# Optimization experiments

Measured on AMD Instinct MI355X. Metric: run time of the kernel, lower is better.

Reference implementation:

```python
import jax, jax.numpy as jnp
import numpy as np

B, T, D, S, H, O = 256, 64, 16, 64, 128, 8

# Tsit5 Butcher tableau (explicit, FSAL; 5th-order solution weights = last stage row)
C_NODES = [0.0, 0.161, 0.327, 0.9, 0.9800255409045097, 1.0, 1.0]
A_TAB = [
    [],
    [0.161],
    [-0.008480655492356989, 0.335480655492357],
    [2.8971530571054935, -6.359448489975075, 4.3622954328695815],
    [5.325864828439257, -11.748883564062828, 7.4955393428898365, -0.09249506636175525],
    [5.86145544294642, -12.92096931784711, 8.159367898576159, -0.071584973281401, -0.028269050394068383],
    [0.09646076681806523, 0.01, 0.4798896504144996, 1.379008574103742, -3.290069515436081, 2.324710524099774],
]
B_SOL = [0.09646076681806523, 0.01, 0.4798896504144996, 1.379008574103742, -3.290069515436081, 2.324710524099774, 0.0]


def setup_inputs() -> dict:
    key = jax.random.key(0)
    ks = jax.random.split(key, 10)
    ts = jnp.linspace(0.0, 1.0, T)
    coeff_d = 0.05 * jax.random.normal(ks[0], (B, T - 1, D), jnp.float32)
    coeff_c = 0.05 * jax.random.normal(ks[1], (B, T - 1, D), jnp.float32)
    coeff_b = 0.2 * jax.random.normal(ks[2], (B, T - 1, D), jnp.float32)
    coeff_a = jax.random.normal(ks[3], (B, T - 1, D), jnp.float32)

    def lin(k, fo, fi):
        s = 1.0 / np.sqrt(fi)
        kw, kb = jax.random.split(k)
        return (jax.random.uniform(kw, (fo, fi), jnp.float32, -s, s),
                jax.random.uniform(kb, (fo,), jnp.float32, -s, s))

    Wi1, bi1 = lin(ks[4], H, D)
    Wi2, bi2 = lin(ks[5], S, H)
    Wf1, bf1 = lin(ks[6], H, S)
    Wf2, bf2 = lin(ks[7], H, H)
    Wf3, bf3 = lin(ks[8], S * D, H)
    Wr, br = lin(ks[9], O, S)
    return dict(ts=ts, coeff_d=coeff_d, coeff_c=coeff_c, coeff_b=coeff_b, coeff_a=coeff_a,
                Wi1=Wi1, bi1=bi1, Wi2=Wi2, bi2=bi2,
                Wf1=Wf1, bf1=bf1, Wf2=Wf2, bf2=bf2, Wf3=Wf3, bf3=bf3, Wr=Wr, br=br)


def _forward(ts, coeff_d, coeff_c, coeff_b, coeff_a,
             Wi1, bi1, Wi2, bi2, Wf1, bf1, Wf2, bf2, Wf3, bf3, Wr, br):
    def vf(y, dxdt):
        # y: (B,S); f(y): (B,S,D) from the MLP (softplus hidden, tanh final); return f(y) @ dx/dt
        h1 = jax.nn.softplus(y @ Wf1.T + bf1)
        h2 = jax.nn.softplus(h1 @ Wf2.T + bf2)
        M = jnp.tanh(h2 @ Wf3.T + bf3).reshape(y.shape[0], S, D)
        return jnp.einsum('bsd,bd->bs', M, dxdt)

    # y0 = initial_mlp(control.evaluate(ts[0])); cubic eval at interval start is coeff_a[:,0]
    x0 = coeff_a[:, 0, :]
    y0 = jax.nn.softplus(x0 @ Wi1.T + bi1) @ Wi2.T + bi2  # (B,S)

    hs = jnp.diff(ts)  # (T-1,)

    def step(y, inp):
        h, cd, cc, cb = inp  # h scalar step size; cd/cc/cb: (B,D) cubic coeffs of this interval
        ks = []
        for j in range(7):
            yj = y
            for m, a in enumerate(A_TAB[j]):
                yj = yj + (h * a) * ks[m]
            frac = C_NODES[j] * h
            dxdt = cb + frac * (2.0 * cc + 3.0 * frac * cd)  # d/dt of cubic interpolation
            ks.append(vf(yj, dxdt))
        y_new = y + h * sum(w * k for w, k in zip(B_SOL, ks))
        return y_new, y_new

    xs = (hs, jnp.swapaxes(coeff_d, 0, 1), jnp.swapaxes(coeff_c, 0, 1), jnp.swapaxes(coeff_b, 0, 1))
    _, ys = jax.lax.scan(step, y0, xs)
    ys = jnp.concatenate([y0[None], ys], axis=0)  # (T,B,S), saved at every ts
    out = ys @ Wr.T + br  # linear readout, identity activation
    return jnp.swapaxes(out, 0, 1)  # (B,T,O)


def reference(ts, coeff_d, coeff_c, coeff_b, coeff_a, Wi1, bi1, Wi2, bi2,
              Wf1, bf1, Wf2, bf2, Wf3, bf3, Wr, br):
    return _forward(ts, coeff_d, coeff_c, coeff_b, coeff_a,
                    Wi1, bi1, Wi2, bi2, Wf1, bf1, Wf2, bf2, Wf3, bf3, Wr, br)
```

## Files before the change

### kernel.cpp

```cpp
#include <hip/hip_runtime.h>
#include <math.h>

typedef _Float16 half_t;
typedef _Float16 half2_t __attribute__((ext_vector_type(2)));
typedef _Float16 half8_t __attribute__((ext_vector_type(8)));
typedef float float4_t __attribute__((ext_vector_type(4)));

#define T_ 64
#define B_ 256
#define D_ 16
#define S_ 64
#define SP_ 68
#define H_ 128
#define O_ 8
#define NSTEP 63
#define NT 512

#define W3_OFF 0
#define W1_OFF 131072
#define W2_OFF 139264
#define WS_HALVES 155648

#define MFMA16(a, b, c) __builtin_amdgcn_mfma_f32_16x16x32_f16(a, b, c, 0, 0, 0)

#if __has_builtin(__builtin_amdgcn_mov_dpp)
#define DPP_ADD(x, ctrl) \
  ((x) + __int_as_float(__builtin_amdgcn_mov_dpp(__float_as_int(x), (ctrl), 0xF, 0xF, true)))
#else
#define DPP_ADD(x, ctrl) ((x) + __shfl_xor((x), (ctrl) == 0xB1 ? 1 : (ctrl) == 0x4E ? 2 : (ctrl) == 0x141 ? 4 : 8))
#endif

__device__ constexpr float AE[6][6] = {
  {0.161f, 0.f, 0.f, 0.f, 0.f, 0.f},
  {-0.008480655492356989f, 0.335480655492357f, 0.f, 0.f, 0.f, 0.f},
  {2.8971530571054935f, -6.359448489975075f, 4.3622954328695815f, 0.f, 0.f, 0.f},
  {5.325864828439257f, -11.748883564062828f, 7.4955393428898365f, -0.09249506636175525f, 0.f, 0.f},
  {5.86145544294642f, -12.92096931784711f, 8.159367898576159f, -0.071584973281401f, -0.028269050394068383f, 0.f},
  {0.09646076681806523f, 0.01f, 0.4798896504144996f, 1.379008574103742f, -3.290069515436081f, 2.324710524099774f}
};
__device__ constexpr float CCn[6] = {0.f, 0.161f, 0.327f, 0.9f, 0.9800255409045097f, 1.f};

__device__ __forceinline__ float softplus_f(float x) {
  return fmaxf(x, 0.f) + __logf(1.f + __expf(-fabsf(x)));
}
__device__ __forceinline__ float tanh_f(float x) {
  float xc = fminf(fmaxf(x, -12.f), 12.f);
  float e = __expf(2.f * xc);
  return (e - 1.f) * __builtin_amdgcn_rcpf(e + 1.f);
}

__global__ __launch_bounds__(256) void convert_kernel(
    const float* __restrict__ Wf1, const float* __restrict__ Wf2,
    const float* __restrict__ Wf3, half_t* __restrict__ wsh)
{
  int q = blockIdx.x * 256 + threadIdx.x;
  if (q < W1_OFF) wsh[q] = (half_t)Wf3[q];
  else if (q < W2_OFF) wsh[q] = (half_t)Wf1[q - W1_OFF];
  else if (q < WS_HALVES) wsh[q] = (half_t)Wf2[q - W2_OFF];
}

__global__ void __launch_bounds__(NT) __attribute__((amdgpu_waves_per_eu(2, 2)))
cde_kernel_mfma(
    const float* __restrict__ ts,
    const float* __restrict__ coeff_d,
    const float* __restrict__ coeff_c,
    const float* __restrict__ coeff_b,
    const float* __restrict__ coeff_a,
    const float* __restrict__ Wi1, const float* __restrict__ bi1,
    const float* __restrict__ Wi2, const float* __restrict__ bi2,
    const float* __restrict__ bf1, const float* __restrict__ bf2,
    const float* __restrict__ bf3,
    const float* __restrict__ Wr, const float* __restrict__ br,
    const half_t* __restrict__ wsh,
    float* __restrict__ out)
{
  __shared__ __align__(16) half_t syj_h[S_];
  __shared__ __align__(16) half_t sh1h[H_];
  __shared__ __align__(16) half_t sh2h[H_];
  __shared__ __align__(16) float shist[T_][SP_];
  __shared__ float sWr[O_ * S_];
  __shared__ float sbr[O_];
  __shared__ float sx0[D_];
  __shared__ float sini[H_];
  __shared__ float shs[T_];

  const int tid = threadIdx.x;
  const int b = blockIdx.x;
  const int w = tid >> 6;
  const int lane = tid & 63;
  const int q = lane >> 4;
  const int c = lane & 15;

  const half_t* __restrict__ w3p = wsh + W3_OFF;
  const half_t* __restrict__ w1p = wsh + W1_OFF;
  const half_t* __restrict__ w2p = wsh + W2_OFF;

  const int n1 = 16 * w + c;
  half8_t bW1[2], bW2[4], bW3[8][4];
  #pragma unroll
  for (int ks = 0; ks < 2; ++ks)
    bW1[ks] = *(const half8_t*)(w1p + n1 * S_ + ks * 32 + q * 8);
  #pragma unroll
  for (int ks = 0; ks < 4; ++ks)
    bW2[ks] = *(const half8_t*)(w2p + n1 * H_ + ks * 32 + q * 8);
  #pragma unroll
  for (int t = 0; t < 8; ++t) {
    const int r = 16 * (8 * w + t) + c;
    #pragma unroll
    for (int ks = 0; ks < 4; ++ks)
      bW3[t][ks] = *(const half8_t*)(w3p + (size_t)r * H_ + ks * 32 + q * 8);
  }
  const float bf1r = bf1[n1];
  const float bf2r = bf2[n1];
  const int s0 = 8 * w + 2 * q;
  const float bf3r0 = bf3[16 * s0 + c];
  const float bf3r1 = bf3[16 * (s0 + 1) + c];

  if (tid < O_ * S_) sWr[tid] = Wr[tid];
  if (tid < O_) sbr[tid] = br[tid];
  if (tid < D_) sx0[tid] = coeff_a[(size_t)b * NSTEP * D_ + tid];
  if (tid < NSTEP) shs[tid] = ts[tid + 1] - ts[tid];
  __syncthreads();
  if (tid < H_) {
    float acc = bi1[tid];
    #pragma unroll
    for (int d = 0; d < D_; ++d) acc += sx0[d] * Wi1[tid * D_ + d];
    sini[tid] = softplus_f(acc);
  }
  __syncthreads();
  if (tid < S_) {
    float acc = bi2[tid];
    for (int h = 0; h < H_; ++h) acc += sini[h] * Wi2[tid * H_ + h];
    shist[0][tid] = acc;
  }
  __syncthreads();

  float yr0 = shist[0][s0];
  float yr1 = shist[0][s0 + 1];
  float kr0[6] = {0.f,0.f,0.f,0.f,0.f,0.f};
  float kr1[6] = {0.f,0.f,0.f,0.f,0.f,0.f};
  if (c == 0) {
    half2_t p; p[0] = (half_t)yr0; p[1] = (half_t)yr1;
    *(half2_t*)(syj_h + s0) = p;
  }
  __syncthreads();

  const float4_t Zv = {0.f, 0.f, 0.f, 0.f};

  for (int t = 0; t < NSTEP; ++t) {
    const float hstep = shs[t];
    const size_t cidx = ((size_t)b * NSTEP + t) * D_ + c;
    const float cbv = coeff_b[cidx];
    const float ccv = coeff_c[cidx];
    const float cdv = coeff_d[cidx];
    float dxj[6];
    #pragma unroll
    for (int j = 0; j < 6; ++j) {
      const float frac = CCn[j] * hstep;
      dxj[j] = cbv + frac * (2.f * ccv + 3.f * frac * cdv);
    }

    #pragma unroll
    for (int j = 0; j < 6; ++j) {
      {
        const half8_t* ap = (const half8_t*)syj_h;
        half8_t a0 = ap[q];
        half8_t a1 = ap[4 + q];
        float4_t acc0 = MFMA16(a0, bW1[0], Zv);
        float4_t acc1 = MFMA16(a1, bW1[1], Zv);
        if (q == 0) sh1h[n1] = (half_t)softplus_f(acc0[0] + acc1[0] + bf1r);
      }
      __syncthreads();

      {
        const half8_t* ap = (const half8_t*)sh1h;
        half8_t a0 = ap[q], a1 = ap[4 + q], a2 = ap[8 + q], a3 = ap[12 + q];
        float4_t accA = MFMA16(a0, bW2[0], Zv);
        float4_t accB = MFMA16(a1, bW2[1], Zv);
        accA = MFMA16(a2, bW2[2], accA);
        accB = MFMA16(a3, bW2[3], accB);
        if (q == 0) sh2h[n1] = (half_t)softplus_f(accA[0] + accB[0] + bf2r);
      }
      __syncthreads();

      {
        const half8_t* ap = (const half8_t*)sh2h;
        half8_t a0 = ap[q], a1 = ap[4 + q], a2 = ap[8 + q], a3 = ap[12 + q];
        float4_t acc3[8];
        #pragma unroll
        for (int tt = 0; tt < 8; ++tt) acc3[tt] = MFMA16(a0, bW3[tt][0], Zv);
        #pragma unroll
        for (int tt = 0; tt < 8; ++tt) acc3[tt] = MFMA16(a1, bW3[tt][1], acc3[tt]);
        #pragma unroll
        for (int tt = 0; tt < 8; ++tt) acc3[tt] = MFMA16(a2, bW3[tt][2], acc3[tt]);
        #pragma unroll
        for (int tt = 0; tt < 8; ++tt) acc3[tt] = MFMA16(a3, bW3[tt][3], acc3[tt]);

        float v0, v1;
        if (q == 0)      { v0 = acc3[0][0]; v1 = acc3[1][0]; }
        else if (q == 1) { v0 = acc3[2][0]; v1 = acc3[3][0]; }
        else if (q == 2) { v0 = acc3[4][0]; v1 = acc3[5][0]; }
        else             { v0 = acc3[6][0]; v1 = acc3[7][0]; }

        const float dx = dxj[j];
        float p0 = tanh_f(v0 + bf3r0) * dx;
        float p1 = tanh_f(v1 + bf3r1) * dx;
        p0 = DPP_ADD(p0, 0xB1);   p1 = DPP_ADD(p1, 0xB1);
        p0 = DPP_ADD(p0, 0x4E);   p1 = DPP_ADD(p1, 0x4E);
        p0 = DPP_ADD(p0, 0x141);  p1 = DPP_ADD(p1, 0x141);
        p0 = DPP_ADD(p0, 0x140);  p1 = DPP_ADD(p1, 0x140);

        kr0[j] = p0;
        kr1[j] = p1;
        float sa0 = AE[j][0] * kr0[0];
        float sa1 = AE[j][0] * kr1[0];
        #pragma unroll
        for (int m = 1; m < 6; ++m) if (m <= j) { sa0 = fmaf(AE[j][m], kr0[m], sa0); sa1 = fmaf(AE[j][m], kr1[m], sa1); }
        float yn0 = fmaf(hstep, sa0, yr0);
        float yn1 = fmaf(hstep, sa1, yr1);
        if (j == 5) { yr0 = yn0; yr1 = yn1; }
        if (c == 0) {
          half2_t p; p[0] = (half_t)yn0; p[1] = (half_t)yn1;
          *(half2_t*)(syj_h + s0) = p;
          if (j == 5) {
            float2 f; f.x = yn0; f.y = yn1;
            *(float2*)(&shist[t + 1][s0]) = f;
          }
        }
      }
      __syncthreads();
    }
  }

  __syncthreads();
  {
    const int tt = tid >> 3;
    const int oo = tid & 7;
    const float4* yp = (const float4*)(&shist[tt][0]);
    const float4* wp = (const float4*)(sWr + oo * S_);
    float a0 = 0.f, a1 = 0.f;
    #pragma unroll
    for (int i = 0; i < 16; i += 2) {
      float4 y0 = yp[i], w0 = wp[i];
      float4 y1 = yp[i + 1], w1 = wp[i + 1];
      a0 += y0.x * w0.x + y0.y * w0.y + y0.z * w0.z + y0.w * w0.w;
      a1 += y1.x * w1.x + y1.y * w1.y + y1.z * w1.z + y1.w * w1.w;
    }
    out[((size_t)b * T_ + tt) * O_ + oo] = a0 + a1 + sbr[oo];
  }
}

extern "C" void kernel_launch(void* const* d_in, const int* in_sizes, int n_in,
                              void* d_out, int out_size, void* d_ws, size_t ws_size,
                              hipStream_t stream) {
  const float* ts  = (const float*)d_in[0];
  const float* cd  = (const float*)d_in[1];
  const float* cc  = (const float*)d_in[2];
  const float* cb  = (const float*)d_in[3];
  const float* ca  = (const float*)d_in[4];
  const float* Wi1 = (const float*)d_in[5];
  const float* bi1 = (const float*)d_in[6];
  const float* Wi2 = (const float*)d_in[7];
  const float* bi2 = (const float*)d_in[8];
  const float* Wf1 = (const float*)d_in[9];
  const float* bf1 = (const float*)d_in[10];
  const float* Wf2 = (const float*)d_in[11];
  const float* bf2 = (const float*)d_in[12];
  const float* Wf3 = (const float*)d_in[13];
  const float* bf3 = (const float*)d_in[14];
  const float* Wr  = (const float*)d_in[15];
  const float* br  = (const float*)d_in[16];

  half_t* wsh = (half_t*)d_ws;
  hipLaunchKernelGGL(convert_kernel, dim3((WS_HALVES + 255) / 256), dim3(256), 0, stream,
                     Wf1, Wf2, Wf3, wsh);
  hipLaunchKernelGGL(cde_kernel_mfma, dim3(B_), dim3(NT), 0, stream,
                     ts, cd, cc, cb, ca, Wi1, bi1, Wi2, bi2,
                     bf1, bf2, bf3, Wr, br, wsh, (float*)d_out);
}
```

Measured before the change: 503.9 us.

## Replace per-row MFMA matvecs with v_dot2 packed-half dot products

Each block handles one batch row, so the MLP matvecs used MFMA tiles where only one row of the 16x16 output was useful. This change computes them with v_dot2_f32_f16 on packed half pairs. Each thread holds weight slices in registers and partial sums are combined with DPP reductions. The aim is to cut the wasted MFMA work and its latency on a strictly serial per-step chain, at the cost of more VALU instructions and a different register footprint.

```diff
diff --git a/kernel.cpp b/kernel.cpp
--- a/kernel.cpp
+++ b/kernel.cpp
@@ -4,7 +4,6 @@
 typedef _Float16 half_t;
 typedef _Float16 half2_t __attribute__((ext_vector_type(2)));
 typedef _Float16 half8_t __attribute__((ext_vector_type(8)));
-typedef float float4_t __attribute__((ext_vector_type(4)));
 
 #define T_ 64
 #define B_ 256
@@ -21,8 +20,6 @@
 #define W2_OFF 139264
 #define WS_HALVES 155648
 
-#define MFMA16(a, b, c) __builtin_amdgcn_mfma_f32_16x16x32_f16(a, b, c, 0, 0, 0)
-
 #if __has_builtin(__builtin_amdgcn_mov_dpp)
 #define DPP_ADD(x, ctrl) \
   ((x) + __int_as_float(__builtin_amdgcn_mov_dpp(__float_as_int(x), (ctrl), 0xF, 0xF, true)))
@@ -49,6 +46,13 @@
   return (e - 1.f) * __builtin_amdgcn_rcpf(e + 1.f);
 }
 
+__device__ __forceinline__ float dot2f(half2_t a, half2_t b, float acc) {
+  float af = __builtin_bit_cast(float, a);
+  float bf = __builtin_bit_cast(float, b);
+  asm("v_dot2_f32_f16 %0, %1, %2, %0" : "+v"(acc) : "v"(af), "v"(bf));
+  return acc;
+}
+
 __global__ __launch_bounds__(256) void convert_kernel(
     const float* __restrict__ Wf1, const float* __restrict__ Wf2,
     const float* __restrict__ Wf3, half_t* __restrict__ wsh)
@@ -60,7 +64,7 @@
 }
 
 __global__ void __launch_bounds__(NT) __attribute__((amdgpu_waves_per_eu(2, 2)))
-cde_kernel_mfma(
+cde_kernel_dot2(
     const float* __restrict__ ts,
     const float* __restrict__ coeff_d,
     const float* __restrict__ coeff_c,
@@ -90,29 +94,35 @@
   const int lane = tid & 63;
   const int q = lane >> 4;
   const int c = lane & 15;
+  const int o1 = tid >> 2;
+  const int kc1 = tid & 3;
+  const int khalf = c & 1;
+  const int s0 = 8 * w + 2 * q;
 
   const half_t* __restrict__ w3p = wsh + W3_OFF;
   const half_t* __restrict__ w1p = wsh + W1_OFF;
   const half_t* __restrict__ w2p = wsh + W2_OFF;
 
-  const int n1 = 16 * w + c;
-  half8_t bW1[2], bW2[4], bW3[8][4];
-  #pragma unroll
-  for (int ks = 0; ks < 2; ++ks)
-    bW1[ks] = *(const half8_t*)(w1p + n1 * S_ + ks * 32 + q * 8);
-  #pragma unroll
-  for (int ks = 0; ks < 4; ++ks)
-    bW2[ks] = *(const half8_t*)(w2p + n1 * H_ + ks * 32 + q * 8);
-  #pragma unroll
-  for (int t = 0; t < 8; ++t) {
-    const int r = 16 * (8 * w + t) + c;
-    #pragma unroll
-    for (int ks = 0; ks < 4; ++ks)
-      bW3[t][ks] = *(const half8_t*)(w3p + (size_t)r * H_ + ks * 32 + q * 8);
-  }
-  const float bf1r = bf1[n1];
-  const float bf2r = bf2[n1];
-  const int s0 = 8 * w + 2 * q;
+  __align__(16) half2_t w1v[8], w2v[16], w3v[4][32];
+  {
+    const half8_t* p1 = (const half8_t*)(w1p + o1 * S_ + kc1 * 16);
+    ((half8_t*)w1v)[0] = p1[0];
+    ((half8_t*)w1v)[1] = p1[1];
+    const half8_t* p2 = (const half8_t*)(w2p + o1 * H_ + kc1 * 32);
+    #pragma unroll
+    for (int i = 0; i < 4; ++i) ((half8_t*)w2v)[i] = p2[i];
+    const int ce = c & 14;
+    const int rows[4] = {16 * s0 + ce, 16 * (s0 + 1) + ce,
+                         16 * s0 + ce + 1, 16 * (s0 + 1) + ce + 1};
+    #pragma unroll
+    for (int r = 0; r < 4; ++r) {
+      const half8_t* p3 = (const half8_t*)(w3p + (size_t)rows[r] * H_ + khalf * 64);
+      #pragma unroll
+      for (int i = 0; i < 8; ++i) ((half8_t*)&w3v[r][0])[i] = p3[i];
+    }
+  }
+  const float bf1v = bf1[o1];
+  const float bf2v = bf2[o1];
   const float bf3r0 = bf3[16 * s0 + c];
   const float bf3r1 = bf3[16 * (s0 + 1) + c];
 
@@ -145,64 +155,77 @@
   }
   __syncthreads();
 
-  const float4_t Zv = {0.f, 0.f, 0.f, 0.f};
-
   for (int t = 0; t < NSTEP; ++t) {
     const float hstep = shs[t];
     const size_t cidx = ((size_t)b * NSTEP + t) * D_ + c;
     const float cbv = coeff_b[cidx];
     const float ccv = coeff_c[cidx];
     const float cdv = coeff_d[cidx];
-    float dxj[6];
-    #pragma unroll
-    for (int j = 0; j < 6; ++j) {
-      const float frac = CCn[j] * hstep;
-      dxj[j] = cbv + frac * (2.f * ccv + 3.f * frac * cdv);
-    }
 
     #pragma unroll
     for (int j = 0; j < 6; ++j) {
       {
-        const half8_t* ap = (const half8_t*)syj_h;
-        half8_t a0 = ap[q];
-        half8_t a1 = ap[4 + q];
-        float4_t acc0 = MFMA16(a0, bW1[0], Zv);
-        float4_t acc1 = MFMA16(a1, bW1[1], Zv);
-        if (q == 0) sh1h[n1] = (half_t)softplus_f(acc0[0] + acc1[0] + bf1r);
+        __align__(16) half2_t y2v[8];
+        const half8_t* yp = (const half8_t*)syj_h + kc1 * 2;
+        ((half8_t*)y2v)[0] = yp[0];
+        ((half8_t*)y2v)[1] = yp[1];
+        float a0 = 0.f, a1 = 0.f;
+        #pragma unroll
+        for (int i = 0; i < 4; ++i) {
+          a0 = dot2f(w1v[i], y2v[i], a0);
+          a1 = dot2f(w1v[i + 4], y2v[i + 4], a1);
+        }
+        float v = a0 + a1;
+        v = DPP_ADD(v, 0xB1);
+        v = DPP_ADD(v, 0x4E);
+        if (kc1 == 0) sh1h[o1] = (half_t)softplus_f(v + bf1v);
       }
       __syncthreads();
 
       {
-        const half8_t* ap = (const half8_t*)sh1h;
-        half8_t a0 = ap[q], a1 = ap[4 + q], a2 = ap[8 + q], a3 = ap[12 + q];
-        float4_t accA = MFMA16(a0, bW2[0], Zv);
-        float4_t accB = MFMA16(a1, bW2[1], Zv);
-        accA = MFMA16(a2, bW2[2], accA);
-        accB = MFMA16(a3, bW2[3], accB);
-        if (q == 0) sh2h[n1] = (half_t)softplus_f(accA[0] + accB[0] + bf2r);
+        __align__(16) half2_t h1v[16];
+        const half8_t* hp = (const half8_t*)sh1h + kc1 * 4;
+        #pragma unroll
+        for (int i = 0; i < 4; ++i) ((half8_t*)h1v)[i] = hp[i];
+        float a0 = 0.f, a1 = 0.f;
+        #pragma unroll
+        for (int i = 0; i < 8; ++i) {
+          a0 = dot2f(w2v[i], h1v[i], a0);
+          a1 = dot2f(w2v[i + 8], h1v[i + 8], a1);
+        }
+        float v = a0 + a1;
+        v = DPP_ADD(v, 0xB1);
+        v = DPP_ADD(v, 0x4E);
+        if (kc1 == 0) sh2h[o1] = (half_t)softplus_f(v + bf2v);
       }
       __syncthreads();
 
       {
-        const half8_t* ap = (const half8_t*)sh2h;
-        half8_t a0 = ap[q], a1 = ap[4 + q], a2 = ap[8 + q], a3 = ap[12 + q];
-        float4_t acc3[8];
-        #pragma unroll
-        for (int tt = 0; tt < 8; ++tt) acc3[tt] = MFMA16(a0, bW3[tt][0], Zv);
-        #pragma unroll
-        for (int tt = 0; tt < 8; ++tt) acc3[tt] = MFMA16(a1, bW3[tt][1], acc3[tt]);
-        #pragma unroll
-        for (int tt = 0; tt < 8; ++tt) acc3[tt] = MFMA16(a2, bW3[tt][2], acc3[tt]);
-        #pragma unroll
-        for (int tt = 0; tt < 8; ++tt) acc3[tt] = MFMA16(a3, bW3[tt][3], acc3[tt]);
-
-        float v0, v1;
-        if (q == 0)      { v0 = acc3[0][0]; v1 = acc3[1][0]; }
-        else if (q == 1) { v0 = acc3[2][0]; v1 = acc3[3][0]; }
-        else if (q == 2) { v0 = acc3[4][0]; v1 = acc3[5][0]; }
-        else             { v0 = acc3[6][0]; v1 = acc3[7][0]; }
-
-        const float dx = dxj[j];
+        __align__(16) half2_t h2v[32];
+        const half8_t* hp = (const half8_t*)sh2h + khalf * 8;
+        #pragma unroll
+        for (int i = 0; i < 8; ++i) ((half8_t*)h2v)[i] = hp[i];
+
+        float pa[4][2] = {{0.f,0.f},{0.f,0.f},{0.f,0.f},{0.f,0.f}};
+        #pragma unroll
+        for (int i = 0; i < 16; ++i) {
+          #pragma unroll
+          for (int r = 0; r < 4; ++r) {
+            pa[r][0] = dot2f(w3v[r][2 * i],     h2v[2 * i],     pa[r][0]);
+            pa[r][1] = dot2f(w3v[r][2 * i + 1], h2v[2 * i + 1], pa[r][1]);
+          }
+        }
+        float vf[4];
+        #pragma unroll
+        for (int r = 0; r < 4; ++r) {
+          float s = pa[r][0] + pa[r][1];
+          vf[r] = DPP_ADD(s, 0xB1);
+        }
+        const float v0 = khalf ? vf[2] : vf[0];
+        const float v1 = khalf ? vf[3] : vf[1];
+
+        const float frac = CCn[j] * hstep;
+        const float dx = cbv + frac * (2.f * ccv + 3.f * frac * cdv);
         float p0 = tanh_f(v0 + bf3r0) * dx;
         float p1 = tanh_f(v1 + bf3r1) * dx;
         p0 = DPP_ADD(p0, 0xB1);   p1 = DPP_ADD(p1, 0xB1);
@@ -274,7 +297,7 @@
   half_t* wsh = (half_t*)d_ws;
   hipLaunchKernelGGL(convert_kernel, dim3((WS_HALVES + 255) / 256), dim3(256), 0, stream,
                      Wf1, Wf2, Wf3, wsh);
-  hipLaunchKernelGGL(cde_kernel_mfma, dim3(B_), dim3(NT), 0, stream,
+  hipLaunchKernelGGL(cde_kernel_dot2, dim3(B_), dim3(NT), 0, stream,
                      ts, cd, cc, cb, ca, Wi1, bi1, Wi2, bi2,
                      bf1, bf2, bf3, Wr, br, wsh, (float*)d_out);
 }
```

New measurement: 612.1 us. 21.5% more time.
